# Kernel optimization log

Hardware: AMD Instinct MI355X
Metric: run time of the kernel (lower is better)

Reference implementation:

```python
import jax, jax.numpy as jnp
import numpy as np

N = 100000
E = 1600000
D_IN = 64
D_HID = 64
D_OUT = 64


def setup_inputs() -> dict:
    key = jax.random.key(0)
    ks = jax.random.split(key, 9)
    x = jax.random.normal(ks[0], (N, D_IN), dtype=jnp.float32)
    edge_index = jax.random.randint(ks[1], (2, E), 0, N, dtype=jnp.int64)
    s1 = 1.0 / np.sqrt(D_IN)
    s2 = 1.0 / np.sqrt(D_HID)
    # PyG SAGEConv: lin_l (applied to aggregated neighbors, has bias), lin_r (root, no bias)
    W1_l = jax.random.uniform(ks[2], (D_HID, D_IN), jnp.float32, -s1, s1)
    b1 = jax.random.uniform(ks[3], (D_HID,), jnp.float32, -s1, s1)
    W1_r = jax.random.uniform(ks[4], (D_HID, D_IN), jnp.float32, -s1, s1)
    W2_l = jax.random.uniform(ks[5], (D_OUT, D_HID), jnp.float32, -s2, s2)
    b2 = jax.random.uniform(ks[6], (D_OUT,), jnp.float32, -s2, s2)
    W2_r = jax.random.uniform(ks[7], (D_OUT, D_HID), jnp.float32, -s2, s2)
    return {"x": x, "edge_index": edge_index, "W1_l": W1_l, "b1": b1, "W1_r": W1_r,
            "W2_l": W2_l, "b2": b2, "W2_r": W2_r}


def _sage_conv(x, src, dst, W_l, b, W_r, n_nodes):
    # mean aggregation of source features at destination nodes
    deg = jax.ops.segment_sum(jnp.ones(src.shape[0], x.dtype), dst, num_segments=n_nodes)
    agg = jax.ops.segment_sum(x[src], dst, num_segments=n_nodes)  # [N, d]
    agg = agg / jnp.maximum(deg, 1.0)[:, None]
    return agg @ W_l.T + b + x @ W_r.T


def reference(x, edge_index, W1_l, b1, W1_r, W2_l, b2, W2_r):
    src, dst = edge_index[0], edge_index[1]
    h = jax.nn.relu(_sage_conv(x, src, dst, W1_l, b1, W1_r, N))
    out = _sage_conv(h, src, dst, W2_l, b2, W2_r, N)
    return out
```

## Files before the change

### kernel.cpp

```cpp
#include <hip/hip_runtime.h>
#include <hip/hip_fp16.h>

#define D 64
#define IDXCAP 448
#define NB1 256

typedef _Float16 f16;
typedef _Float16 f16x8 __attribute__((ext_vector_type(8)));
typedef float f32x4 __attribute__((ext_vector_type(4)));

__device__ __forceinline__ float4 h4_to_f4(uint2 u) {
    float2 fa = __half22float2(__builtin_bit_cast(__half2, u.x));
    float2 fb = __half22float2(__builtin_bit_cast(__half2, u.y));
    return make_float4(fa.x, fa.y, fb.x, fb.y);
}


__global__ __launch_bounds__(256) void p1_count_convert(
        const int* __restrict__ dst, int E, int chunk, int* __restrict__ mat, int bshift,
        const float* __restrict__ x, f16* __restrict__ xh, int n4) {
    __shared__ int h[NB1];
    h[threadIdx.x] = 0;
    __syncthreads();
    int k = blockIdx.x;
    int e0 = k * chunk;
    int e1 = min(E, e0 + chunk);
    for (int e = e0 + threadIdx.x; e < e1; e += 256)
        atomicAdd(&h[dst[e] >> bshift], 1);
    __syncthreads();
    mat[k * NB1 + threadIdx.x] = h[threadIdx.x];
    int t = blockIdx.x * 256 + threadIdx.x;
    int stride = gridDim.x * 256;
    for (int i = t; i < n4; i += stride) {
        float4 v = ((const float4*)x)[i];
        uint2 o;
        o.x = __builtin_bit_cast(unsigned int, __float22half2_rn(make_float2(v.x, v.y)));
        o.y = __builtin_bit_cast(unsigned int, __float22half2_rn(make_float2(v.z, v.w)));
        ((uint2*)xh)[i] = o;
    }
}

__global__ __launch_bounds__(256) void p1_scan(int* __restrict__ mat, int* __restrict__ bucketBase,
                                               int* __restrict__ rowptr, int N, int E) {
    __shared__ int sc[NB1];
    int b = threadIdx.x;
    int tot = 0;
    for (int k = 0; k < NB1; ++k) tot += mat[k * NB1 + b];
    sc[b] = tot;
    __syncthreads();
    for (int off = 1; off < NB1; off <<= 1) {
        int add = (b >= off) ? sc[b - off] : 0;
        __syncthreads();
        sc[b] += add;
        __syncthreads();
    }
    int base = sc[b] - tot;
    bucketBase[b] = base;
    if (b == 0) { bucketBase[NB1] = E; rowptr[N] = E; }
    int run = base;
    for (int k = 0; k < NB1; ++k) {
        int v = mat[k * NB1 + b];
        mat[k * NB1 + b] = run;
        run += v;
    }
}

__global__ __launch_bounds__(256) void p2_scatter(
        const int* __restrict__ src, const int* __restrict__ dst, int E, int chunk,
        const int* __restrict__ mat, int bshift, int2* __restrict__ pairs) {
    __shared__ int cur[NB1];
    int k = blockIdx.x;
    cur[threadIdx.x] = mat[k * NB1 + threadIdx.x];
    __syncthreads();
    int e0 = k * chunk;
    int e1 = min(E, e0 + chunk);
    for (int e = e0 + threadIdx.x; e < e1; e += 256) {
        int d = dst[e], s = src[e];
        int pos = atomicAdd(&cur[d >> bshift], 1);
        pairs[pos] = make_int2(d, s);
    }
}

__global__ __launch_bounds__(256) void p3_build(
        const int2* __restrict__ pairs, const int* __restrict__ bucketBase, int bshift,
        int* __restrict__ rowptr, int* __restrict__ csr, int N) {
    __shared__ int hist[1024];
    __shared__ int cur[1024];
    __shared__ int part[256];
    int b = blockIdx.x;
    int npb = 1 << bshift;
    int nb0 = b << bshift;
    int nn = min(N - nb0, npb);
    int e0 = bucketBase[b], e1 = bucketBase[b + 1];
    for (int i = threadIdx.x; i < nn; i += 256) hist[i] = 0;
    __syncthreads();
    for (int e = e0 + threadIdx.x; e < e1; e += 256)
        atomicAdd(&hist[pairs[e].x - nb0], 1);
    __syncthreads();
    int R = (nn + 255) >> 8;
    int t = threadIdx.x;
    int base_i = t * R;
    int lsum = 0;
    for (int r = 0; r < R; ++r) { int i = base_i + r; if (i < nn) lsum += hist[i]; }
    part[t] = lsum;
    __syncthreads();
    for (int off = 1; off < 256; off <<= 1) {
        int add = (t >= off) ? part[t - off] : 0;
        __syncthreads();
        part[t] += add;
        __syncthreads();
    }
    int run = e0 + (part[t] - lsum);
    for (int r = 0; r < R; ++r) {
        int i = base_i + r;
        if (i < nn) {
            int v = hist[i];
            rowptr[nb0 + i] = run;
            cur[i] = run;
            run += v;
        }
    }
    __syncthreads();
    for (int e = e0 + threadIdx.x; e < e1; e += 256) {
        int2 p = pairs[e];
        int pos = atomicAdd(&cur[p.x - nb0], 1);
        csr[pos] = p.y;
    }
}

#define GATHER_BODY(IP)                                                          \
    for (; j + 16 <= deg; j += 16) {                                             \
        int s0 = (IP)[j + r4];                                                   \
        int s1 = (IP)[j + 4 + r4];                                               \
        int s2 = (IP)[j + 8 + r4];                                               \
        int s3 = (IP)[j + 12 + r4];                                              \
        float4 g0 = h4_to_f4(xh2[(size_t)s0 * 16 + f8]);                         \
        float4 g1 = h4_to_f4(xh2[(size_t)s1 * 16 + f8]);                         \
        float4 g2 = h4_to_f4(xh2[(size_t)s2 * 16 + f8]);                         \
        float4 g3 = h4_to_f4(xh2[(size_t)s3 * 16 + f8]);                         \
        acc.x += (g0.x + g1.x) + (g2.x + g3.x);                                  \
        acc.y += (g0.y + g1.y) + (g2.y + g3.y);                                  \
        acc.z += (g0.z + g1.z) + (g2.z + g3.z);                                  \
        acc.w += (g0.w + g1.w) + (g2.w + g3.w);                                  \
    }                                                                            \
    if (j + 8 <= deg) {                                                          \
        int s0 = (IP)[j + r4];                                                   \
        int s1 = (IP)[j + 4 + r4];                                               \
        float4 g0 = h4_to_f4(xh2[(size_t)s0 * 16 + f8]);                         \
        float4 g1 = h4_to_f4(xh2[(size_t)s1 * 16 + f8]);                         \
        acc.x += g0.x + g1.x; acc.y += g0.y + g1.y;                              \
        acc.z += g0.z + g1.z; acc.w += g0.w + g1.w;                              \
        j += 8;                                                                  \
    }                                                                            \
    for (; j < deg; j += 4) {                                                    \
        int jj = j + r4;                                                         \
        if (jj < deg) {                                                          \
            float4 g = h4_to_f4(xh2[(size_t)(IP)[jj] * 16 + f8]);                \
            acc.x += g.x; acc.y += g.y; acc.z += g.z; acc.w += g.w;              \
        }                                                                        \
    }

template<int RELU, int OUT16>
__global__ __launch_bounds__(512, 4) void sage_mfma(
        const f16* __restrict__ xh, const int* __restrict__ rowptr,
        const int* __restrict__ csr,
        const float* __restrict__ Wl, const float* __restrict__ bias,
        const float* __restrict__ Wr,
        f16* __restrict__ out16, float* __restrict__ out32, int n_nodes) {
    __shared__ __align__(16) f16 sB[16 * 512];
    __shared__ __align__(16) f16 sA[8][16 * 72];
    __shared__ int sIdx[8][IDXCAP];

    for (int u = threadIdx.x; u < 16 * 64; u += blockDim.x) {
        int f = u >> 6;
        int l = u & 63;
        int t = f >> 2, q = f & 3;
        const float* Wsel = (q < 2) ? Wl : Wr;
        int d  = t * 16 + (l & 15);
        int k0 = (q & 1) * 32 + (l >> 4) * 8;
        const float4* wp = (const float4*)(Wsel + d * 64 + k0);
        float4 w0 = wp[0], w1 = wp[1];
        uint4 pk;
        pk.x = __builtin_bit_cast(unsigned int, __float22half2_rn(make_float2(w0.x, w0.y)));
        pk.y = __builtin_bit_cast(unsigned int, __float22half2_rn(make_float2(w0.z, w0.w)));
        pk.z = __builtin_bit_cast(unsigned int, __float22half2_rn(make_float2(w1.x, w1.y)));
        pk.w = __builtin_bit_cast(unsigned int, __float22half2_rn(make_float2(w1.z, w1.w)));
        *(uint4*)&sB[f * 512 + l * 8] = pk;
    }
    __syncthreads();

    const int lane = threadIdx.x & 63;
    const int wid  = threadIdx.x >> 6;
    const int r4   = lane >> 4;
    const int f8   = lane & 15;
    f16* myA = &sA[wid][0];
    int* myIdx = &sIdx[wid][0];

    float bias_t[4];
    #pragma unroll
    for (int t = 0; t < 4; ++t) bias_t[t] = bias[t * 16 + f8];

    const int wavesPerBlock = blockDim.x >> 6;
    const int gwave = blockIdx.x * wavesPerBlock + wid;
    const int nwaves = gridDim.x * wavesPerBlock;
    const uint2* __restrict__ xh2 = (const uint2*)xh;

    for (int nb = gwave * 16; nb < n_nodes; nb += nwaves * 16) {
        int rpl = 0;
        {
            int ii = nb + lane;
            if (lane < 17) rpl = rowptr[ii < n_nodes ? ii : n_nodes];
        }
        int rbase = __builtin_amdgcn_readlane(rpl, 0);
        int rend  = __builtin_amdgcn_readlane(rpl, 16);
        int cnt = rend - rbase;
        bool useLds = (cnt <= IDXCAP);

        if (useLds) {
            for (int c = lane; c < cnt; c += 64)
                myIdx[c] = csr[rbase + c];
        }

        int rn = nb + f8; if (rn >= n_nodes) rn = n_nodes - 1;
        const f16x8* rrow = (const f16x8*)(xh + (size_t)rn * 64);
        f16x8 a2 = rrow[r4];
        f16x8 a3 = rrow[4 + r4];

        #pragma unroll 1
        for (int i = 0; i < 16; ++i) {
            int r0 = __builtin_amdgcn_readlane(rpl, i);
            int r1 = __builtin_amdgcn_readlane(rpl, i + 1);
            int deg = r1 - r0;
            float4 acc = make_float4(0.f, 0.f, 0.f, 0.f);
            int j = 0;
            if (useLds) {
                const int* ip = myIdx + (r0 - rbase);
                GATHER_BODY(ip)
            } else {
                const int* ip = csr + r0;
                GATHER_BODY(ip)
            }
            acc.x += __shfl_xor(acc.x, 16, 64);
            acc.y += __shfl_xor(acc.y, 16, 64);
            acc.z += __shfl_xor(acc.z, 16, 64);
            acc.w += __shfl_xor(acc.w, 16, 64);
            acc.x += __shfl_xor(acc.x, 32, 64);
            acc.y += __shfl_xor(acc.y, 32, 64);
            acc.z += __shfl_xor(acc.z, 32, 64);
            acc.w += __shfl_xor(acc.w, 32, 64);
            float iv = 1.0f / (float)(deg > 0 ? deg : 1);
            if (r4 == (i & 3)) {
                uint2 w;
                w.x = __builtin_bit_cast(unsigned int,
                        __float22half2_rn(make_float2(acc.x * iv, acc.y * iv)));
                w.y = __builtin_bit_cast(unsigned int,
                        __float22half2_rn(make_float2(acc.z * iv, acc.w * iv)));
                *(uint2*)&myA[i * 72 + f8 * 4] = w;
            }
        }

        f16x8 a0 = *(const f16x8*)&myA[f8 * 72 + r4 * 8];
        f16x8 a1 = *(const f16x8*)&myA[f8 * 72 + 32 + r4 * 8];

        #pragma unroll
        for (int t = 0; t < 4; ++t) {
            f32x4 c = {0.f, 0.f, 0.f, 0.f};
            c = __builtin_amdgcn_mfma_f32_16x16x32_f16(a0, *(const f16x8*)&sB[(t*4+0)*512 + lane*8], c, 0, 0, 0);
            c = __builtin_amdgcn_mfma_f32_16x16x32_f16(a1, *(const f16x8*)&sB[(t*4+1)*512 + lane*8], c, 0, 0, 0);
            c = __builtin_amdgcn_mfma_f32_16x16x32_f16(a2, *(const f16x8*)&sB[(t*4+2)*512 + lane*8], c, 0, 0, 0);
            c = __builtin_amdgcn_mfma_f32_16x16x32_f16(a3, *(const f16x8*)&sB[(t*4+3)*512 + lane*8], c, 0, 0, 0);
            #pragma unroll
            for (int rr = 0; rr < 4; ++rr) {
                int n = nb + r4 * 4 + rr;
                if (n < n_nodes) {
                    float v = c[rr] + bias_t[t];
                    if (RELU) v = fmaxf(v, 0.f);
                    if (OUT16) out16[(size_t)n * 64 + t * 16 + f8] = (f16)v;
                    else       out32[(size_t)n * 64 + t * 16 + f8] = v;
                }
            }
        }
    }
}


__global__ void count_rank_convert_kernel(const int* __restrict__ dst, int* __restrict__ counts,
                                          int* __restrict__ rank, int E,
                                          const float* __restrict__ x, f16* __restrict__ xh, int n4) {
    int t = blockIdx.x * blockDim.x + threadIdx.x;
    int stride = gridDim.x * blockDim.x;
    int E4 = E >> 2;
    for (int e4 = t; e4 < E4; e4 += stride) {
        int4 d = ((const int4*)dst)[e4];
        int4 rk;
        rk.x = atomicAdd(&counts[d.x], 1);
        rk.y = atomicAdd(&counts[d.y], 1);
        rk.z = atomicAdd(&counts[d.z], 1);
        rk.w = atomicAdd(&counts[d.w], 1);
        ((int4*)rank)[e4] = rk;
    }
    for (int e = (E & ~3) + t; e < E; e += stride)
        rank[e] = atomicAdd(&counts[dst[e]], 1);
    for (int i = t; i < n4; i += stride) {
        float4 v = ((const float4*)x)[i];
        uint2 o;
        o.x = __builtin_bit_cast(unsigned int, __float22half2_rn(make_float2(v.x, v.y)));
        o.y = __builtin_bit_cast(unsigned int, __float22half2_rn(make_float2(v.z, v.w)));
        ((uint2*)xh)[i] = o;
    }
}

__global__ void scan_block_sums(const int* __restrict__ counts, int* __restrict__ partial, int N4) {
    __shared__ int sd[256];
    int idx = blockIdx.x * 256 + threadIdx.x;
    int s = 0;
    if (idx < N4) {
        int4 v = ((const int4*)counts)[idx];
        s = v.x + v.y + v.z + v.w;
    }
    sd[threadIdx.x] = s; __syncthreads();
    for (int off = 128; off > 0; off >>= 1) {
        if (threadIdx.x < off) sd[threadIdx.x] += sd[threadIdx.x + off];
        __syncthreads();
    }
    if (threadIdx.x == 0) partial[blockIdx.x] = sd[0];
}

__global__ void scan_partials(const int* __restrict__ partial, int* __restrict__ pscan,
                              int* __restrict__ rowptr, int NB, int N, int E) {
    if (threadIdx.x == 0 && blockIdx.x == 0) {
        int s = 0;
        for (int i = 0; i < NB; ++i) { pscan[i] = s; s += partial[i]; }
        rowptr[N] = E;
    }
}

__global__ void scan_final(const int* __restrict__ counts, const int* __restrict__ pscan,
                           int* __restrict__ rowptr, int N4) {
    __shared__ int sc[256];
    int idx = blockIdx.x * 256 + threadIdx.x;
    int4 v = make_int4(0, 0, 0, 0);
    if (idx < N4) v = ((const int4*)counts)[idx];
    int msum = v.x + v.y + v.z + v.w;
    sc[threadIdx.x] = msum; __syncthreads();
    for (int off = 1; off < 256; off <<= 1) {
        int add = (threadIdx.x >= (unsigned)off) ? sc[threadIdx.x - off] : 0;
        __syncthreads();
        sc[threadIdx.x] += add;
        __syncthreads();
    }
    int excl = sc[threadIdx.x] - msum + pscan[blockIdx.x];
    if (idx < N4) {
        int4 r;
        r.x = excl;
        r.y = excl + v.x;
        r.z = r.y + v.y;
        r.w = r.z + v.z;
        ((int4*)rowptr)[idx] = r;
    }
}

__global__ void fill_csr2(const int* __restrict__ src, const int* __restrict__ dst,
                          const int* __restrict__ rowptr, const int* __restrict__ rank,
                          int* __restrict__ csr, int E) {
    int t = blockIdx.x * blockDim.x + threadIdx.x;
    int stride = gridDim.x * blockDim.x;
    int E4 = E >> 2;
    for (int e4 = t; e4 < E4; e4 += stride) {
        int4 d = ((const int4*)dst)[e4];
        int4 rk = ((const int4*)rank)[e4];
        int4 s = ((const int4*)src)[e4];
        csr[rowptr[d.x] + rk.x] = s.x;
        csr[rowptr[d.y] + rk.y] = s.y;
        csr[rowptr[d.z] + rk.z] = s.z;
        csr[rowptr[d.w] + rk.w] = s.w;
    }
    for (int e = (E & ~3) + t; e < E; e += stride)
        csr[rowptr[dst[e]] + rank[e]] = src[e];
}


extern "C" void kernel_launch(void* const* d_in, const int* in_sizes, int n_in,
                              void* d_out, int out_size, void* d_ws, size_t ws_size,
                              hipStream_t stream) {
    const float* x   = (const float*)d_in[0];
    const int*   ei  = (const int*)d_in[1];
    const float* W1l = (const float*)d_in[2];
    const float* b1  = (const float*)d_in[3];
    const float* W1r = (const float*)d_in[4];
    const float* W2l = (const float*)d_in[5];
    const float* b2  = (const float*)d_in[6];
    const float* W2r = (const float*)d_in[7];
    float* out = (float*)d_out;

    const int N = in_sizes[0] / D;
    const int E = in_sizes[1] / 2;
    const int* src = ei;
    const int* dst = ei + E;

    int wavesNeeded = (N + 15) / 16;
    int blocks = (wavesNeeded + 7) / 8;

    int bshift = 0;
    while ((1 << bshift) <= 1024 && ((N + (1 << bshift) - 1) >> bshift) > NB1) ++bshift;
    bool bok = ((1 << bshift) <= 1024) && (((N + (1 << bshift) - 1) >> bshift) <= NB1);
    int nbuck = bok ? ((N + (1 << bshift) - 1) >> bshift) : 0;

    {
        size_t off = 0;
        auto alloc = [&](size_t bytes) { size_t r = off; off += (bytes + 511) & ~(size_t)511; return r; };
        size_t o_mat    = alloc((size_t)NB1 * NB1 * 4);
        size_t o_bb     = alloc((size_t)(NB1 + 1) * 4);
        size_t o_pairs  = alloc((size_t)E * 8);
        size_t o_rowptr = alloc((size_t)(N + 1) * 4);
        size_t o_csr    = alloc((size_t)E * 4);
        size_t o_xh     = alloc((size_t)N * D * 2);
        size_t o_hh     = alloc((size_t)N * D * 2);

        if (bok && E >= 1 && off <= ws_size) {
            int*  mat    = (int*)((char*)d_ws + o_mat);
            int*  bb     = (int*)((char*)d_ws + o_bb);
            int2* pairs  = (int2*)((char*)d_ws + o_pairs);
            int*  rowptr = (int*)((char*)d_ws + o_rowptr);
            int*  csr    = (int*)((char*)d_ws + o_csr);
            f16*  xh     = (f16*)((char*)d_ws + o_xh);
            f16*  hh     = (f16*)((char*)d_ws + o_hh);

            int chunk = (E + NB1 - 1) / NB1;
            p1_count_convert<<<NB1, 256, 0, stream>>>(dst, E, chunk, mat, bshift, x, xh, N * D / 4);
            p1_scan<<<1, 256, 0, stream>>>(mat, bb, rowptr, N, E);
            p2_scatter<<<NB1, 256, 0, stream>>>(src, dst, E, chunk, mat, bshift, pairs);
            p3_build<<<nbuck, 256, 0, stream>>>(pairs, bb, bshift, rowptr, csr, N);

            sage_mfma<1, 1><<<blocks, 512, 0, stream>>>(xh, rowptr, csr, W1l, b1, W1r, hh, nullptr, N);
            sage_mfma<0, 0><<<blocks, 512, 0, stream>>>(hh, rowptr, csr, W2l, b2, W2r, nullptr, out, N);
            return;
        }
    }

    const int N4 = N / 4;
    const int NB = (N4 + 255) / 256;
    size_t off = 0;
    auto alloc = [&](size_t bytes) { size_t r = off; off += (bytes + 511) & ~(size_t)511; return r; };
    size_t f_counts = alloc((size_t)N * 4);
    size_t f_rowptr = alloc((size_t)(N + 1) * 4);
    size_t f_part   = alloc((size_t)NB * 4);
    size_t f_pscan  = alloc((size_t)NB * 4);
    size_t f_csr    = alloc((size_t)E * 4);
    size_t f_xh     = alloc((size_t)N * D * 2);
    size_t f_hh     = alloc((size_t)N * D * 2);

    int* counts  = (int*)((char*)d_ws + f_counts);
    int* rowptr  = (int*)((char*)d_ws + f_rowptr);
    int* partial = (int*)((char*)d_ws + f_part);
    int* pscan   = (int*)((char*)d_ws + f_pscan);
    int* csr     = (int*)((char*)d_ws + f_csr);
    f16* xh      = (f16*)((char*)d_ws + f_xh);
    f16* hh      = (f16*)((char*)d_ws + f_hh);
    int* rank    = (int*)hh;

    hipMemsetAsync(counts, 0, (size_t)N * 4, stream);
    count_rank_convert_kernel<<<2048, 256, 0, stream>>>(dst, counts, rank, E, x, xh, N * D / 4);
    scan_block_sums<<<NB, 256, 0, stream>>>(counts, partial, N4);
    scan_partials<<<1, 64, 0, stream>>>(partial, pscan, rowptr, NB, N, E);
    scan_final<<<NB, 256, 0, stream>>>(counts, pscan, rowptr, N4);
    fill_csr2<<<2048, 256, 0, stream>>>(src, dst, rowptr, rank, csr, E);

    sage_mfma<1, 1><<<blocks, 512, 0, stream>>>(xh, rowptr, csr, W1l, b1, W1r, hh, nullptr, N);
    sage_mfma<0, 0><<<blocks, 512, 0, stream>>>(hh, rowptr, csr, W2l, b2, W2r, nullptr, out, N);
}
```

Before: 177.0 us.

## Software-pipeline neighbor gathers across destination rows with double-buffered registers

Restructures the per-row gather loop so that up to 32 neighbor feature rows for the next destination node are loaded into registers while the current node's loads are being summed, using two register buffers (uA/uB). Rows with more than 32 neighbors fall back to the old gather loop for the remainder. The index staging into LDS is also split into an unrolled load phase followed by a store phase. The aim is to keep more memory loads in flight and hide gather latency, at the cost of higher register pressure, which may hurt occupancy under the 512x4 launch bounds. Padded lanes for low-degree nodes also issue redundant clamped loads.

```diff
diff --git a/kernel.cpp b/kernel.cpp
--- a/kernel.cpp
+++ b/kernel.cpp
@@ -127,6 +127,7 @@
         csr[pos] = p.y;
     }
 }
+
 
 #define GATHER_BODY(IP)                                                          \
     for (; j + 16 <= deg; j += 16) {                                             \
@@ -160,6 +161,57 @@
         }                                                                        \
     }
 
+#define BUTTERFLY(acc)                                                           \
+    acc.x += __shfl_xor(acc.x, 16, 64);                                          \
+    acc.y += __shfl_xor(acc.y, 16, 64);                                          \
+    acc.z += __shfl_xor(acc.z, 16, 64);                                          \
+    acc.w += __shfl_xor(acc.w, 16, 64);                                          \
+    acc.x += __shfl_xor(acc.x, 32, 64);                                          \
+    acc.y += __shfl_xor(acc.y, 32, 64);                                          \
+    acc.z += __shfl_xor(acc.z, 32, 64);                                          \
+    acc.w += __shfl_xor(acc.w, 32, 64);
+
+#define VLOAD(UU, IP, DEG)                                                       \
+    if ((DEG) > 0) {                                                             \
+        _Pragma("unroll")                                                        \
+        for (int u = 0; u < 8; ++u) {                                            \
+            int e = 4 * u + r4;                                                  \
+            int ec = e < (DEG) ? e : (DEG) - 1;                                  \
+            int sx = (IP)[ec];                                                   \
+            uint2 tv = xh2[(size_t)sx * 16 + f8];                                \
+            if (e >= (DEG)) { tv.x = 0u; tv.y = 0u; }                            \
+            UU[u] = tv;                                                          \
+        }                                                                        \
+    }
+
+#define CONSUME(UU, DG, IPX, I)                                                  \
+    {                                                                            \
+        float4 acc = make_float4(0.f, 0.f, 0.f, 0.f);                            \
+        if ((DG) > 0) {                                                          \
+            _Pragma("unroll")                                                    \
+            for (int u = 0; u < 8; ++u) {                                        \
+                float4 g = h4_to_f4(UU[u]);                                      \
+                acc.x += g.x; acc.y += g.y; acc.z += g.z; acc.w += g.w;          \
+            }                                                                    \
+        }                                                                        \
+        if ((DG) > 32) {                                                         \
+            int j = 32; int deg = (DG); const int* ip = (IPX);                   \
+            GATHER_BODY(ip)                                                      \
+        }                                                                        \
+        BUTTERFLY(acc)                                                           \
+        float iv = 1.0f / (float)((DG) > 0 ? (DG) : 1);                          \
+        if (r4 == ((I) & 3)) {                                                   \
+            uint2 w;                                                             \
+            w.x = __builtin_bit_cast(unsigned int,                               \
+                    __float22half2_rn(make_float2(acc.x * iv, acc.y * iv)));     \
+            w.y = __builtin_bit_cast(unsigned int,                               \
+                    __float22half2_rn(make_float2(acc.z * iv, acc.w * iv)));     \
+            *(uint2*)&myA[(I) * 72 + f8 * 4] = w;                                \
+        }                                                                        \
+    }
+
+#define RL(X) __builtin_amdgcn_readlane(rpl, (X))
+
 template<int RELU, int OUT16>
 __global__ __launch_bounds__(512, 4) void sage_mfma(
         const f16* __restrict__ xh, const int* __restrict__ rowptr,
@@ -211,52 +263,57 @@
             int ii = nb + lane;
             if (lane < 17) rpl = rowptr[ii < n_nodes ? ii : n_nodes];
         }
-        int rbase = __builtin_amdgcn_readlane(rpl, 0);
-        int rend  = __builtin_amdgcn_readlane(rpl, 16);
+        int rbase = RL(0);
+        int rend  = RL(16);
         int cnt = rend - rbase;
         bool useLds = (cnt <= IDXCAP);
 
         if (useLds) {
-            for (int c = lane; c < cnt; c += 64)
-                myIdx[c] = csr[rbase + c];
+            int tmp[7];
+            #pragma unroll
+            for (int u = 0; u < 7; ++u) {
+                int c = lane + 64 * u;
+                tmp[u] = (c < cnt) ? csr[rbase + c] : 0;
+            }
+            #pragma unroll
+            for (int u = 0; u < 7; ++u) {
+                int c = lane + 64 * u;
+                if (c < cnt) myIdx[c] = tmp[u];
+            }
         }
+
+        const int* ibase = useLds ? (const int*)myIdx : csr;
+        const int  roff  = useLds ? rbase : 0;
 
         int rn = nb + f8; if (rn >= n_nodes) rn = n_nodes - 1;
         const f16x8* rrow = (const f16x8*)(xh + (size_t)rn * 64);
         f16x8 a2 = rrow[r4];
         f16x8 a3 = rrow[4 + r4];
 
+        uint2 uA[8], uB[8];
+        int rpA = RL(0);
+        int rpB = RL(1);
+        int dgA = rpB - rpA;
+        const int* ipA = ibase + (rpA - roff);
+        VLOAD(uA, ipA, dgA)
+
         #pragma unroll 1
-        for (int i = 0; i < 16; ++i) {
-            int r0 = __builtin_amdgcn_readlane(rpl, i);
-            int r1 = __builtin_amdgcn_readlane(rpl, i + 1);
-            int deg = r1 - r0;
-            float4 acc = make_float4(0.f, 0.f, 0.f, 0.f);
-            int j = 0;
-            if (useLds) {
-                const int* ip = myIdx + (r0 - rbase);
-                GATHER_BODY(ip)
-            } else {
-                const int* ip = csr + r0;
-                GATHER_BODY(ip)
+        for (int p = 0; p < 8; ++p) {
+            const int i0 = 2 * p, i1 = 2 * p + 1;
+            int rpC = RL(i1 + 1);
+            int dgB = rpC - rpB;
+            const int* ipB = ibase + (rpB - roff);
+            VLOAD(uB, ipB, dgB)
+            CONSUME(uA, dgA, ipA, i0)
+            int dgA2 = 0; const int* ipA2 = ipA; int rpD = rpC;
+            if (p < 7) {
+                rpD = RL(i1 + 2);
+                dgA2 = rpD - rpC;
+                ipA2 = ibase + (rpC - roff);
+                VLOAD(uA, ipA2, dgA2)
             }
-            acc.x += __shfl_xor(acc.x, 16, 64);
-            acc.y += __shfl_xor(acc.y, 16, 64);
-            acc.z += __shfl_xor(acc.z, 16, 64);
-            acc.w += __shfl_xor(acc.w, 16, 64);
-            acc.x += __shfl_xor(acc.x, 32, 64);
-            acc.y += __shfl_xor(acc.y, 32, 64);
-            acc.z += __shfl_xor(acc.z, 32, 64);
-            acc.w += __shfl_xor(acc.w, 32, 64);
-            float iv = 1.0f / (float)(deg > 0 ? deg : 1);
-            if (r4 == (i & 3)) {
-                uint2 w;
-                w.x = __builtin_bit_cast(unsigned int,
-                        __float22half2_rn(make_float2(acc.x * iv, acc.y * iv)));
-                w.y = __builtin_bit_cast(unsigned int,
-                        __float22half2_rn(make_float2(acc.z * iv, acc.w * iv)));
-                *(uint2*)&myA[i * 72 + f8 * 4] = w;
-            }
+            CONSUME(uB, dgB, ipB, i1)
+            dgA = dgA2; ipA = ipA2; rpB = rpD;
         }
 
         f16x8 a0 = *(const f16x8*)&myA[f8 * 72 + r4 * 8];
```

Result: slower. 275.9 us (+55.9%).

## Parallelize CSR-build scan, double chunks and buckets, cache pairs in registers

Applied to the files above, without the earlier changes.

Replaces the single-block bucket scan with a three-kernel parallel scan (per-bucket totals, bucket prefix, per-bucket column scan) over a transposed count matrix. Edge chunks and destination buckets go from 256 to 512 each, so the scatter and build phases have more blocks and smaller per-bucket node ranges. p3_build keeps each thread's pairs in registers between the histogram pass and the placement pass, which avoids reading the pairs array twice. The cost is two extra kernel launches and higher register pressure in p3_build.

```diff
diff --git a/kernel.cpp b/kernel.cpp
--- a/kernel.cpp
+++ b/kernel.cpp
@@ -3,7 +3,9 @@
 
 #define D 64
 #define IDXCAP 448
-#define NB1 256
+#define NCH 512
+#define MAXB 512
+#define RMAX 20
 
 typedef _Float16 f16;
 typedef _Float16 f16x8 __attribute__((ext_vector_type(8)));
@@ -19,8 +21,8 @@
 __global__ __launch_bounds__(256) void p1_count_convert(
         const int* __restrict__ dst, int E, int chunk, int* __restrict__ mat, int bshift,
         const float* __restrict__ x, f16* __restrict__ xh, int n4) {
-    __shared__ int h[NB1];
-    h[threadIdx.x] = 0;
+    __shared__ int h[MAXB];
+    for (int i = threadIdx.x; i < MAXB; i += 256) h[i] = 0;
     __syncthreads();
     int k = blockIdx.x;
     int e0 = k * chunk;
@@ -28,7 +30,8 @@
     for (int e = e0 + threadIdx.x; e < e1; e += 256)
         atomicAdd(&h[dst[e] >> bshift], 1);
     __syncthreads();
-    mat[k * NB1 + threadIdx.x] = h[threadIdx.x];
+    for (int b = threadIdx.x; b < MAXB; b += 256)
+        mat[b * NCH + k] = h[b];
     int t = blockIdx.x * 256 + threadIdx.x;
     int stride = gridDim.x * 256;
     for (int i = t; i < n4; i += stride) {
@@ -40,37 +43,64 @@
     }
 }
 
-__global__ __launch_bounds__(256) void p1_scan(int* __restrict__ mat, int* __restrict__ bucketBase,
-                                               int* __restrict__ rowptr, int N, int E) {
-    __shared__ int sc[NB1];
-    int b = threadIdx.x;
-    int tot = 0;
-    for (int k = 0; k < NB1; ++k) tot += mat[k * NB1 + b];
-    sc[b] = tot;
-    __syncthreads();
-    for (int off = 1; off < NB1; off <<= 1) {
-        int add = (b >= off) ? sc[b - off] : 0;
-        __syncthreads();
-        sc[b] += add;
-        __syncthreads();
-    }
-    int base = sc[b] - tot;
-    bucketBase[b] = base;
-    if (b == 0) { bucketBase[NB1] = E; rowptr[N] = E; }
-    int run = base;
-    for (int k = 0; k < NB1; ++k) {
-        int v = mat[k * NB1 + b];
-        mat[k * NB1 + b] = run;
-        run += v;
-    }
+__global__ __launch_bounds__(256) void scan_bt(const int* __restrict__ mat, int* __restrict__ tot) {
+    __shared__ int sd[256];
+    int b = blockIdx.x;
+    int s = 0;
+    for (int k = threadIdx.x; k < NCH; k += 256) s += mat[b * NCH + k];
+    sd[threadIdx.x] = s; __syncthreads();
+    for (int off = 128; off > 0; off >>= 1) {
+        if (threadIdx.x < off) sd[threadIdx.x] += sd[threadIdx.x + off];
+        __syncthreads();
+    }
+    if (threadIdx.x == 0) tot[b] = sd[0];
+}
+
+__global__ __launch_bounds__(512) void scan_tot(const int* __restrict__ tot, int* __restrict__ bucketBase,
+                                                int* __restrict__ rowptr, int nbuck, int N, int E) {
+    __shared__ int sc[MAXB];
+    int t = threadIdx.x;
+    int v = (t < nbuck) ? tot[t] : 0;
+    sc[t] = v;
+    __syncthreads();
+    for (int off = 1; off < MAXB; off <<= 1) {
+        int add = (t >= off) ? sc[t - off] : 0;
+        __syncthreads();
+        sc[t] += add;
+        __syncthreads();
+    }
+    if (t < nbuck) bucketBase[t] = sc[t] - v;
+    if (t == 0) { bucketBase[nbuck] = E; rowptr[N] = E; }
+}
+
+__global__ __launch_bounds__(256) void scan_col(int* __restrict__ mat, const int* __restrict__ bucketBase) {
+    __shared__ int part[256];
+    int b = blockIdx.x;
+    int base = bucketBase[b];
+    int t = threadIdx.x;
+    int l0 = mat[b * NCH + 2 * t];
+    int l1 = mat[b * NCH + 2 * t + 1];
+    int lsum = l0 + l1;
+    part[t] = lsum;
+    __syncthreads();
+    for (int off = 1; off < 256; off <<= 1) {
+        int add = (t >= off) ? part[t - off] : 0;
+        __syncthreads();
+        part[t] += add;
+        __syncthreads();
+    }
+    int excl = base + part[t] - lsum;
+    mat[b * NCH + 2 * t] = excl;
+    mat[b * NCH + 2 * t + 1] = excl + l0;
 }
 
 __global__ __launch_bounds__(256) void p2_scatter(
         const int* __restrict__ src, const int* __restrict__ dst, int E, int chunk,
         const int* __restrict__ mat, int bshift, int2* __restrict__ pairs) {
-    __shared__ int cur[NB1];
+    __shared__ int cur[MAXB];
     int k = blockIdx.x;
-    cur[threadIdx.x] = mat[k * NB1 + threadIdx.x];
+    for (int b = threadIdx.x; b < MAXB; b += 256)
+        cur[b] = mat[b * NCH + k];
     __syncthreads();
     int e0 = k * chunk;
     int e1 = min(E, e0 + chunk);
@@ -92,13 +122,27 @@
     int nb0 = b << bshift;
     int nn = min(N - nb0, npb);
     int e0 = bucketBase[b], e1 = bucketBase[b + 1];
-    for (int i = threadIdx.x; i < nn; i += 256) hist[i] = 0;
-    __syncthreads();
-    for (int e = e0 + threadIdx.x; e < e1; e += 256)
-        atomicAdd(&hist[pairs[e].x - nb0], 1);
+    int cnt = e1 - e0;
+    int t = threadIdx.x;
+    for (int i = t; i < npb; i += 256) hist[i] = 0;
+    __syncthreads();
+    bool reg = (cnt <= 256 * RMAX);
+    int2 v[RMAX];
+    if (reg) {
+        #pragma unroll
+        for (int r = 0; r < RMAX; ++r) {
+            int e = e0 + r * 256 + t;
+            if (e < e1) {
+                v[r] = pairs[e];
+                atomicAdd(&hist[v[r].x - nb0], 1);
+            }
+        }
+    } else {
+        for (int e = e0 + t; e < e1; e += 256)
+            atomicAdd(&hist[pairs[e].x - nb0], 1);
+    }
     __syncthreads();
     int R = (nn + 255) >> 8;
-    int t = threadIdx.x;
     int base_i = t * R;
     int lsum = 0;
     for (int r = 0; r < R; ++r) { int i = base_i + r; if (i < nn) lsum += hist[i]; }
@@ -114,17 +158,28 @@
     for (int r = 0; r < R; ++r) {
         int i = base_i + r;
         if (i < nn) {
-            int v = hist[i];
+            int hv = hist[i];
             rowptr[nb0 + i] = run;
             cur[i] = run;
-            run += v;
-        }
-    }
-    __syncthreads();
-    for (int e = e0 + threadIdx.x; e < e1; e += 256) {
-        int2 p = pairs[e];
-        int pos = atomicAdd(&cur[p.x - nb0], 1);
-        csr[pos] = p.y;
+            run += hv;
+        }
+    }
+    __syncthreads();
+    if (reg) {
+        #pragma unroll
+        for (int r = 0; r < RMAX; ++r) {
+            int e = e0 + r * 256 + t;
+            if (e < e1) {
+                int pos = atomicAdd(&cur[v[r].x - nb0], 1);
+                csr[pos] = v[r].y;
+            }
+        }
+    } else {
+        for (int e = e0 + t; e < e1; e += 256) {
+            int2 p = pairs[e];
+            int pos = atomicAdd(&cur[p.x - nb0], 1);
+            csr[pos] = p.y;
+        }
     }
 }
 
@@ -402,15 +457,16 @@
     int blocks = (wavesNeeded + 7) / 8;
 
     int bshift = 0;
-    while ((1 << bshift) <= 1024 && ((N + (1 << bshift) - 1) >> bshift) > NB1) ++bshift;
-    bool bok = ((1 << bshift) <= 1024) && (((N + (1 << bshift) - 1) >> bshift) <= NB1);
+    while ((1 << bshift) <= 1024 && ((N + (1 << bshift) - 1) >> bshift) > MAXB) ++bshift;
+    bool bok = ((1 << bshift) <= 1024) && (((N + (1 << bshift) - 1) >> bshift) <= MAXB);
     int nbuck = bok ? ((N + (1 << bshift) - 1) >> bshift) : 0;
 
     {
         size_t off = 0;
         auto alloc = [&](size_t bytes) { size_t r = off; off += (bytes + 511) & ~(size_t)511; return r; };
-        size_t o_mat    = alloc((size_t)NB1 * NB1 * 4);
-        size_t o_bb     = alloc((size_t)(NB1 + 1) * 4);
+        size_t o_mat    = alloc((size_t)MAXB * NCH * 4);
+        size_t o_tot    = alloc((size_t)MAXB * 4);
+        size_t o_bb     = alloc((size_t)(MAXB + 1) * 4);
         size_t o_pairs  = alloc((size_t)E * 8);
         size_t o_rowptr = alloc((size_t)(N + 1) * 4);
         size_t o_csr    = alloc((size_t)E * 4);
@@ -419,6 +475,7 @@
 
         if (bok && E >= 1 && off <= ws_size) {
             int*  mat    = (int*)((char*)d_ws + o_mat);
+            int*  tot    = (int*)((char*)d_ws + o_tot);
             int*  bb     = (int*)((char*)d_ws + o_bb);
             int2* pairs  = (int2*)((char*)d_ws + o_pairs);
             int*  rowptr = (int*)((char*)d_ws + o_rowptr);
@@ -426,10 +483,12 @@
             f16*  xh     = (f16*)((char*)d_ws + o_xh);
             f16*  hh     = (f16*)((char*)d_ws + o_hh);
 
-            int chunk = (E + NB1 - 1) / NB1;
-            p1_count_convert<<<NB1, 256, 0, stream>>>(dst, E, chunk, mat, bshift, x, xh, N * D / 4);
-            p1_scan<<<1, 256, 0, stream>>>(mat, bb, rowptr, N, E);
-            p2_scatter<<<NB1, 256, 0, stream>>>(src, dst, E, chunk, mat, bshift, pairs);
+            int chunk = (E + NCH - 1) / NCH;
+            p1_count_convert<<<NCH, 256, 0, stream>>>(dst, E, chunk, mat, bshift, x, xh, N * D / 4);
+            scan_bt<<<nbuck, 256, 0, stream>>>(mat, tot);
+            scan_tot<<<1, 512, 0, stream>>>(tot, bb, rowptr, nbuck, N, E);
+            scan_col<<<nbuck, 256, 0, stream>>>(mat, bb);
+            p2_scatter<<<NCH, 256, 0, stream>>>(src, dst, E, chunk, mat, bshift, pairs);
             p3_build<<<nbuck, 256, 0, stream>>>(pairs, bb, bshift, rowptr, csr, N);
 
             sage_mfma<1, 1><<<blocks, 512, 0, stream>>>(xh, rowptr, csr, W1l, b1, W1r, hh, nullptr, N);
```

Measured after the change: 163.2 us. 1.08x faster.
